# Kernel tuning notes

Hardware: AMD Instinct MI355X
Metric: run time of the kernel (lower is better)

The kernel has to match this reference:

```python
import jax, jax.numpy as jnp
import numpy as np

ACT_BIT = 3
W_BIT = 2


def fake_quant(x, bits):
    """Symmetric uniform fake-quantization to `bits` bits (dequantized values)."""
    qmax = float((1 << (bits - 1)) - 1)
    scale = jnp.max(jnp.abs(x)) / qmax
    scale = jnp.where(scale == 0, jnp.ones_like(scale), scale)
    return jnp.clip(jnp.round(x / scale), -qmax, qmax) * scale


def setup_inputs() -> dict:
    key = jax.random.key(0)
    kA, kX, kWi, kWo = jax.random.split(key, 4)
    N, D_IN, D_H, D_OUT = 8192, 128, 64, 16
    A = jax.random.normal(kA, (N, N), dtype=jnp.float32)       # dense subgraph adjacency (binarized inside)
    X = jax.random.normal(kX, (N, D_IN), dtype=jnp.float32)    # node features
    W_in = jax.random.normal(kWi, (D_IN, D_H), dtype=jnp.float32)
    W_out = jax.random.normal(kWo, (D_H, D_OUT), dtype=jnp.float32)
    return {"A": A, "X": X, "W_in": W_in, "W_out": W_out}


def reference(A, X, W_in, W_out):
    # QGTC GCNConv_Qnt: A quantized to 1 bit, activations to act_bit, weights to w_bit.
    Aq = (A > 0).astype(A.dtype)                 # 1-bit adjacency (bit_qnt(A, 1))
    Xq = fake_quant(X, ACT_BIT)                  # X_Qnt
    Wi = fake_quant(W_in, W_BIT)                 # weight_Qnt
    Wo = fake_quant(W_out, W_BIT)
    # Layer 1: mm_v1(X, W_in) then mm_v1(A, .) with output re-quantized to act_bit
    h = Aq @ (Xq @ Wi)                           # [N, D_H]
    hq = fake_quant(h, ACT_BIT)
    # Layer 2 (output layer)
    out = Aq @ (hq @ Wo)                         # [N, D_OUT]
    return out
```

## Files before the change

### kernel.cpp

```cpp
#include <hip/hip_runtime.h>

#define NN 8192
#define DIN 128
#define DH 64
#define DOUT 16
#define KS 16

typedef _Float16 half8 __attribute__((ext_vector_type(8)));
typedef float f32x4 __attribute__((ext_vector_type(4)));

#define OFF_SC    0u
#define OFF_PART  256u
#define OFF_WIQ   2048u
#define OFF_WOQ   34816u
#define OFF_YT    65536u
#define OFF_RT    1114112u
#define OFF_HF    1376256u
#define OFF_BITS  3473408u
#define OFF_P1    11862016u
#define OFF_P2    45416448u

__device__ __forceinline__ float getscale(const unsigned* sc, int idx, float qmax) {
  float s = __uint_as_float(sc[idx]) / qmax;
  return (s == 0.0f) ? 1.0f : s;
}

__device__ __forceinline__ half8 expand8(unsigned bb) {
  uint4 w;
  w.x = ((bb & 1u)  ? 0x3C00u : 0u) | ((bb & 2u)   ? 0x3C000000u : 0u);
  w.y = ((bb & 4u)  ? 0x3C00u : 0u) | ((bb & 8u)   ? 0x3C000000u : 0u);
  w.z = ((bb & 16u) ? 0x3C00u : 0u) | ((bb & 32u)  ? 0x3C000000u : 0u);
  w.w = ((bb & 64u) ? 0x3C00u : 0u) | ((bb & 128u) ? 0x3C000000u : 0u);
  return __builtin_bit_cast(half8, w);
}

__global__ __launch_bounds__(256) void k_scales(const float* __restrict__ X,
                                                const float* __restrict__ Wi,
                                                const float* __restrict__ Wo,
                                                unsigned* part) {
  __shared__ float red[256];
  int t = threadIdx.x, b = blockIdx.x;
  float m = 0.0f;
  if (b < 240) {
    for (int i = b * 256 + t; i < NN * DIN; i += 240 * 256) m = fmaxf(m, fabsf(X[i]));
  } else if (b == 240) {
    for (int i = t; i < DIN * DH; i += 256) m = fmaxf(m, fabsf(Wi[i]));
  } else {
    for (int i = t; i < DH * DOUT; i += 256) m = fmaxf(m, fabsf(Wo[i]));
  }
  red[t] = m; __syncthreads();
  for (int s = 128; s > 0; s >>= 1) {
    if (t < s) red[t] = fmaxf(red[t], red[t + s]);
    __syncthreads();
  }
  if (t == 0) part[b] = __float_as_uint(red[0]);
}

__global__ __launch_bounds__(256) void k_quantW(const float* __restrict__ Wi,
                                                const float* __restrict__ Wo,
                                                const unsigned* __restrict__ part,
                                                unsigned* sc,
                                                float* __restrict__ Wiq,
                                                float* __restrict__ Woq) {
  __shared__ float red[256];
  int t = threadIdx.x;
  red[t] = (t < 240) ? __uint_as_float(part[t]) : 0.0f;
  __syncthreads();
  for (int s = 128; s > 0; s >>= 1) {
    if (t < s) red[t] = fmaxf(red[t], red[t + s]);
    __syncthreads();
  }
  if (t == 0) {
    sc[0] = __float_as_uint(red[0]);
    sc[1] = part[240];
    sc[2] = part[241];
    sc[3] = 0u;
  }
  float swi = __uint_as_float(part[240]); swi = (swi == 0.0f) ? 1.0f : swi;
  float swo = __uint_as_float(part[241]); swo = (swo == 0.0f) ? 1.0f : swo;
  for (int i = t; i < DIN * DH; i += 256) {
    float q = rintf(Wi[i] / swi);
    Wiq[i] = fminf(fmaxf(q, -1.0f), 1.0f);
  }
  for (int i = t; i < DH * DOUT; i += 256) {
    float q = rintf(Wo[i] / swo);
    Woq[i] = fminf(fmaxf(q, -1.0f), 1.0f);
  }
}

__global__ __launch_bounds__(256) void k_bitsY(const float* __restrict__ A,
                                               const float* __restrict__ X,
                                               const float* __restrict__ Wiq,
                                               const unsigned* __restrict__ sc,
                                               unsigned char* __restrict__ bits,
                                               _Float16* __restrict__ YT) {
  __shared__ float Xs[8][129];
  __shared__ float Ws[DIN][DH];
  const int t = threadIdx.x, bx = blockIdx.x;
  if (bx < 4096) {
    const int lane = t & 63, warp = t >> 6;
    const size_t wbase = ((size_t)bx * 4 + warp) * 4096;
    const float* ap = A + wbase + lane;
    unsigned char* bp = bits + (wbase >> 3);
    const int l8 = lane & 7;
#pragma unroll
    for (int g = 0; g < 8; ++g) {
      float x0 = ap[g * 512 + 0 * 64];
      float x1 = ap[g * 512 + 1 * 64];
      float x2 = ap[g * 512 + 2 * 64];
      float x3 = ap[g * 512 + 3 * 64];
      float x4 = ap[g * 512 + 4 * 64];
      float x5 = ap[g * 512 + 5 * 64];
      float x6 = ap[g * 512 + 6 * 64];
      float x7 = ap[g * 512 + 7 * 64];
      unsigned long long m0 = __ballot(x0 > 0.0f);
      unsigned long long m1 = __ballot(x1 > 0.0f);
      unsigned long long m2 = __ballot(x2 > 0.0f);
      unsigned long long m3 = __ballot(x3 > 0.0f);
      unsigned long long m4 = __ballot(x4 > 0.0f);
      unsigned long long m5 = __ballot(x5 > 0.0f);
      unsigned long long m6 = __ballot(x6 > 0.0f);
      unsigned long long m7 = __ballot(x7 > 0.0f);
      unsigned long long mine = m0;
      mine = (l8 == 1) ? m1 : mine;
      mine = (l8 == 2) ? m2 : mine;
      mine = (l8 == 3) ? m3 : mine;
      mine = (l8 == 4) ? m4 : mine;
      mine = (l8 == 5) ? m5 : mine;
      mine = (l8 == 6) ? m6 : mine;
      mine = (l8 == 7) ? m7 : mine;
      if (lane < 8) *(unsigned long long*)(bp + g * 64 + l8 * 8) = mine;
    }
    return;
  }
  float sx = getscale(sc, 0, 3.0f);
  const int by = bx - 4096;
  const int k0 = by * 8;
  for (int i = t; i < 8 * DIN; i += 256) {
    int r = i >> 7, c = i & 127;
    float q = rintf(X[(size_t)(k0 + r) * DIN + c] / sx);
    Xs[r][c] = fminf(fmaxf(q, -3.0f), 3.0f);
  }
  for (int i = t; i < DIN * DH; i += 256) Ws[i >> 6][i & 63] = Wiq[i];
  __syncthreads();
  const int r = t & 7, jp = t >> 3, j = jp * 2;
  float a0 = 0.0f, a1 = 0.0f;
  for (int n = 0; n < DIN; ++n) {
    float xv = Xs[r][n];
    a0 = fmaf(xv, Ws[n][j], a0);
    a1 = fmaf(xv, Ws[n][j + 1], a1);
  }
  YT[(size_t)j * NN + k0 + r]       = (_Float16)a0;
  YT[(size_t)(j + 1) * NN + k0 + r] = (_Float16)a1;
}

__global__ __launch_bounds__(256) void k_gemm1(const unsigned char* __restrict__ bits,
                                               const _Float16* __restrict__ YT,
                                               float* __restrict__ P1) {
  __shared__ __align__(16) char Bs[64 * 128];
  const int t = threadIdx.x, lane = t & 63, warp = t >> 6;
  const int row0 = blockIdx.x * 128;
  const int split = blockIdx.y;
  const int l15 = lane & 15, lq = lane >> 4;
  const int sh8 = lq * 8;

  f32x4 acc[2][4] = {};

  const int bn = t >> 2, bp = t & 3;
  const _Float16* bsrc = YT + (size_t)bn * NN + split * 512 + bp * 16;
  char* bdst0 = &Bs[bn * 128 + ((bp * 32) ^ ((bn & 7) << 4))];
  char* bdst1 = &Bs[bn * 128 + ((bp * 32 + 16) ^ ((bn & 7) << 4))];

  const unsigned char* brow0 = bits + (size_t)(row0 + warp * 32 + l15) * 1024 + split * 64;
  const unsigned char* brow1 = brow0 + 16 * 1024;

  uint4 breg0 = *(const uint4*)(bsrc);
  uint4 breg1 = *(const uint4*)(bsrc + 8);

  for (int it = 0; it < 8; ++it) {
    __syncthreads();
    *(uint4*)bdst0 = breg0;
    *(uint4*)bdst1 = breg1;
    if (it < 7) {
      breg0 = *(const uint4*)(bsrc + (it + 1) * 64);
      breg1 = *(const uint4*)(bsrc + (it + 1) * 64 + 8);
    }
    uint2 w0 = *(const uint2*)(brow0 + it * 8);
    uint2 w1 = *(const uint2*)(brow1 + it * 8);
    __syncthreads();
#pragma unroll
    for (int kk = 0; kk < 2; ++kk) {
      half8 af0 = expand8(((kk ? w0.y : w0.x) >> sh8) & 0xffu);
      half8 af1 = expand8(((kk ? w1.y : w1.x) >> sh8) & 0xffu);
#pragma unroll
      for (int n = 0; n < 4; ++n) {
        half8 bf = *(const half8*)(&Bs[(n * 16 + l15) * 128 +
                                       ((lq * 16 + kk * 64) ^ ((l15 & 7) << 4))]);
        acc[0][n] = __builtin_amdgcn_mfma_f32_16x16x32_f16(af0, bf, acc[0][n], 0, 0, 0);
        acc[1][n] = __builtin_amdgcn_mfma_f32_16x16x32_f16(af1, bf, acc[1][n], 0, 0, 0);
      }
    }
  }
  const int r4 = lq * 4;
#pragma unroll
  for (int mf = 0; mf < 2; ++mf) {
#pragma unroll
    for (int n = 0; n < 4; ++n) {
#pragma unroll
      for (int i = 0; i < 4; ++i) {
        int rr = row0 + warp * 32 + mf * 16 + r4 + i;
        int cc = n * 16 + l15;
        P1[((size_t)split * NN + rr) * DH + cc] = acc[mf][n][i];
      }
    }
  }
}

__global__ __launch_bounds__(256) void k_h2(const float* __restrict__ P1,
                                            unsigned* sc, float* __restrict__ hf) {
  float sxw = getscale(sc, 0, 3.0f) * getscale(sc, 1, 1.0f);
  int idx = blockIdx.x * 256 + threadIdx.x;
  const float4* p = (const float4*)P1;
  float4 s = {0, 0, 0, 0};
#pragma unroll
  for (int sp = 0; sp < KS; ++sp) {
    float4 v = p[(size_t)sp * (NN * DH / 4) + idx];
    s.x += v.x; s.y += v.y; s.z += v.z; s.w += v.w;
  }
  s.x *= sxw; s.y *= sxw; s.z *= sxw; s.w *= sxw;
  ((float4*)hf)[idx] = s;
  float m = fmaxf(fmaxf(fabsf(s.x), fabsf(s.y)), fmaxf(fabsf(s.z), fabsf(s.w)));
  __shared__ float red[256];
  red[threadIdx.x] = m; __syncthreads();
  for (int st = 128; st > 0; st >>= 1) {
    if (threadIdx.x < st) red[threadIdx.x] = fmaxf(red[threadIdx.x], red[threadIdx.x + st]);
    __syncthreads();
  }
  if (threadIdx.x == 0) atomicMax(&sc[3], __float_as_uint(red[0]));
}

__global__ __launch_bounds__(256) void k_R(const float* __restrict__ hf,
                                           const float* __restrict__ Woq,
                                           const unsigned* __restrict__ sc,
                                           _Float16* __restrict__ RT) {
  __shared__ float WoS[DH][DOUT];
  float sh = getscale(sc, 3, 3.0f);
  int t = threadIdx.x;
  for (int i = t; i < DH * DOUT; i += 256) WoS[i >> 4][i & 15] = Woq[i];
  __syncthreads();
  int i = blockIdx.x * 16 + (t & 15), j = t >> 4;
  const float4* hp = (const float4*)(hf + (size_t)i * DH);
  float acc = 0.0f;
#pragma unroll 4
  for (int nb = 0; nb < 16; ++nb) {
    float4 h4 = hp[nb];
    float q;
    q = fminf(fmaxf(rintf(h4.x / sh), -3.0f), 3.0f); acc = fmaf(q, WoS[nb * 4 + 0][j], acc);
    q = fminf(fmaxf(rintf(h4.y / sh), -3.0f), 3.0f); acc = fmaf(q, WoS[nb * 4 + 1][j], acc);
    q = fminf(fmaxf(rintf(h4.z / sh), -3.0f), 3.0f); acc = fmaf(q, WoS[nb * 4 + 2][j], acc);
    q = fminf(fmaxf(rintf(h4.w / sh), -3.0f), 3.0f); acc = fmaf(q, WoS[nb * 4 + 3][j], acc);
  }
  RT[(size_t)j * NN + i] = (_Float16)acc;
}

__global__ __launch_bounds__(256) void k_gemm2(const unsigned char* __restrict__ bits,
                                               const _Float16* __restrict__ RT,
                                               float* __restrict__ P2) {
  __shared__ __align__(16) char Rs[16 * 1024];
  const int t = threadIdx.x, lane = t & 63, warp = t >> 6;
  const int row0 = blockIdx.x * 64;
  const int split = blockIdx.y;
  const int l15 = lane & 15, lq = lane >> 4;
  const int sh8 = lq * 8;

  {
    const int rr = t >> 4, cb = (t & 15) * 64;
    const uint4* src = (const uint4*)(RT + (size_t)rr * NN + split * 512 + (t & 15) * 32);
    char* base = &Rs[rr * 1024];
    const int sw = (rr & 7) << 4;
#pragma unroll
    for (int u = 0; u < 4; ++u) *(uint4*)(&base[(cb + u * 16) ^ sw]) = src[u];
  }
  __syncthreads();

  const unsigned char* brow = bits + (size_t)(row0 + warp * 16 + l15) * 1024 + split * 64;
  f32x4 acc = {};
  const int rsw = (l15 & 7) << 4;
#pragma unroll
  for (int it = 0; it < 8; ++it) {
    uint2 w = *(const uint2*)(brow + it * 8);
#pragma unroll
    for (int kk = 0; kk < 2; ++kk) {
      half8 af = expand8(((kk ? w.y : w.x) >> sh8) & 0xffu);
      half8 bf = *(const half8*)(&Rs[l15 * 1024 + ((it * 128 + lq * 16 + kk * 64) ^ rsw)]);
      acc = __builtin_amdgcn_mfma_f32_16x16x32_f16(af, bf, acc, 0, 0, 0);
    }
  }
  const int r4 = lq * 4;
#pragma unroll
  for (int i = 0; i < 4; ++i) {
    int rr = row0 + warp * 16 + r4 + i;
    P2[((size_t)split * NN + rr) * DOUT + l15] = acc[i];
  }
}

__global__ __launch_bounds__(256) void k_out(const float* __restrict__ P2,
                                             const unsigned* __restrict__ sc,
                                             float* __restrict__ out) {
  float s = getscale(sc, 3, 3.0f) * getscale(sc, 2, 1.0f);
  int idx = blockIdx.x * 256 + threadIdx.x;
  const float4* p = (const float4*)P2;
  float4 acc = {0, 0, 0, 0};
#pragma unroll
  for (int sp = 0; sp < KS; ++sp) {
    float4 v = p[(size_t)sp * (NN * DOUT / 4) + idx];
    acc.x += v.x; acc.y += v.y; acc.z += v.z; acc.w += v.w;
  }
  acc.x *= s; acc.y *= s; acc.z *= s; acc.w *= s;
  ((float4*)out)[idx] = acc;
}

extern "C" void kernel_launch(void* const* d_in, const int* in_sizes, int n_in,
                              void* d_out, int out_size, void* d_ws, size_t ws_size,
                              hipStream_t stream) {
  const float* A  = (const float*)d_in[0];
  const float* X  = (const float*)d_in[1];
  const float* Wi = (const float*)d_in[2];
  const float* Wo = (const float*)d_in[3];
  char* ws = (char*)d_ws;
  unsigned* sc        = (unsigned*)(ws + OFF_SC);
  unsigned* part      = (unsigned*)(ws + OFF_PART);
  float* Wiq          = (float*)(ws + OFF_WIQ);
  float* Woq          = (float*)(ws + OFF_WOQ);
  _Float16* YT        = (_Float16*)(ws + OFF_YT);
  _Float16* RT        = (_Float16*)(ws + OFF_RT);
  float* hf           = (float*)(ws + OFF_HF);
  unsigned char* bits = (unsigned char*)(ws + OFF_BITS);
  float* P1           = (float*)(ws + OFF_P1);
  float* P2           = (float*)(ws + OFF_P2);
  float* out          = (float*)d_out;

  k_scales<<<242, 256, 0, stream>>>(X, Wi, Wo, part);
  k_quantW<<<1, 256, 0, stream>>>(Wi, Wo, part, sc, Wiq, Woq);
  k_bitsY<<<5120, 256, 0, stream>>>(A, X, Wiq, sc, bits, YT);
  k_gemm1<<<dim3(NN / 128, KS), 256, 0, stream>>>(bits, YT, P1);
  k_h2<<<NN * DH / 1024, 256, 0, stream>>>(P1, sc, hf);
  k_R<<<NN / 16, 256, 0, stream>>>(hf, Woq, sc, RT);
  k_gemm2<<<dim3(NN / 64, KS), 256, 0, stream>>>(bits, RT, P2);
  k_out<<<NN * DOUT / 1024, 256, 0, stream>>>(P2, sc, out);
}
```

Before: 129.9 us.

## Fuse scale/bit-packing passes, vectorize A binarization, drop split-K partials in second GEMM

A's sign-bit packing now runs in the same launch as the absmax scale reduction, using float4 loads with a different bit ordering. To match that ordering, a column permutation (permk) is applied when writing YT and RT. Weight quantization is folded into the consumer kernels, which removes the k_quantW launch and its workspace buffers. The second GEMM now computes a full-K reduction per block, with an intra-block LDS reduction, and writes scaled output directly, which eliminates the P2 partials and the k_out kernel. The first GEMM's split-K is halved, which lowers partial traffic but costs parallelism. The trade is fewer launches and less global traffic against longer per-block K loops and direct global B-fragment loads in gemm2.

```diff
diff --git a/kernel.cpp b/kernel.cpp
--- a/kernel.cpp
+++ b/kernel.cpp
@@ -4,21 +4,23 @@
 #define DIN 128
 #define DH 64
 #define DOUT 16
-#define KS 16
+#define KS 8
 
 typedef _Float16 half8 __attribute__((ext_vector_type(8)));
 typedef float f32x4 __attribute__((ext_vector_type(4)));
 
 #define OFF_SC    0u
 #define OFF_PART  256u
-#define OFF_WIQ   2048u
-#define OFF_WOQ   34816u
 #define OFF_YT    65536u
 #define OFF_RT    1114112u
 #define OFF_HF    1376256u
 #define OFF_BITS  3473408u
 #define OFF_P1    11862016u
-#define OFF_P2    45416448u
+
+__device__ __forceinline__ int permk(int k) {
+  int e = k & 255;
+  return (k & ~255) | (((e & 3) << 6) | (e >> 2));
+}
 
 __device__ __forceinline__ float getscale(const unsigned* sc, int idx, float qmax) {
   float s = __uint_as_float(sc[idx]) / qmax;
@@ -34,17 +36,40 @@
   return __builtin_bit_cast(half8, w);
 }
 
-__global__ __launch_bounds__(256) void k_scales(const float* __restrict__ X,
-                                                const float* __restrict__ Wi,
-                                                const float* __restrict__ Wo,
-                                                unsigned* part) {
+__global__ __launch_bounds__(256) void k_scalesbits(const float* __restrict__ A,
+                                                    const float* __restrict__ X,
+                                                    const float* __restrict__ Wi,
+                                                    const float* __restrict__ Wo,
+                                                    unsigned char* __restrict__ bits,
+                                                    unsigned* part, unsigned* sc) {
+  const int t = threadIdx.x, bx = blockIdx.x;
+  if (bx < 4096) {
+    const int lane = t & 63, warp = t >> 6;
+    const size_t wbase = ((size_t)bx * 4 + warp) * 4096;
+    const float4* ap = (const float4*)(A + wbase) + lane;
+    unsigned char* bp = bits + (wbase >> 3);
+#pragma unroll
+    for (int g = 0; g < 16; ++g) {
+      float4 v = ap[g * 64];
+      unsigned long long m0 = __ballot(v.x > 0.0f);
+      unsigned long long m1 = __ballot(v.y > 0.0f);
+      unsigned long long m2 = __ballot(v.z > 0.0f);
+      unsigned long long m3 = __ballot(v.w > 0.0f);
+      unsigned long long lo = (lane & 1) ? m1 : m0;
+      unsigned long long hi = (lane & 1) ? m3 : m2;
+      unsigned long long word = (lane & 2) ? hi : lo;
+      if (lane < 4) *(unsigned long long*)(bp + g * 32 + lane * 8) = word;
+    }
+    return;
+  }
   __shared__ float red[256];
-  int t = threadIdx.x, b = blockIdx.x;
+  const int b = bx - 4096;
   float m = 0.0f;
   if (b < 240) {
     for (int i = b * 256 + t; i < NN * DIN; i += 240 * 256) m = fmaxf(m, fabsf(X[i]));
   } else if (b == 240) {
     for (int i = t; i < DIN * DH; i += 256) m = fmaxf(m, fabsf(Wi[i]));
+    if (t == 0) sc[3] = 0u;
   } else {
     for (int i = t; i < DH * DOUT; i += 256) m = fmaxf(m, fabsf(Wo[i]));
   }
@@ -56,92 +81,36 @@
   if (t == 0) part[b] = __float_as_uint(red[0]);
 }
 
-__global__ __launch_bounds__(256) void k_quantW(const float* __restrict__ Wi,
-                                                const float* __restrict__ Wo,
-                                                const unsigned* __restrict__ part,
-                                                unsigned* sc,
-                                                float* __restrict__ Wiq,
-                                                float* __restrict__ Woq) {
+__global__ __launch_bounds__(256) void k_Y(const float* __restrict__ X,
+                                           const float* __restrict__ Wi,
+                                           const unsigned* __restrict__ part,
+                                           unsigned* sc,
+                                           _Float16* __restrict__ YT) {
   __shared__ float red[256];
-  int t = threadIdx.x;
+  __shared__ float Xs[8][129];
+  __shared__ float Ws[DIN][DH];
+  const int t = threadIdx.x;
   red[t] = (t < 240) ? __uint_as_float(part[t]) : 0.0f;
   __syncthreads();
   for (int s = 128; s > 0; s >>= 1) {
     if (t < s) red[t] = fmaxf(red[t], red[t + s]);
     __syncthreads();
   }
-  if (t == 0) {
-    sc[0] = __float_as_uint(red[0]);
-    sc[1] = part[240];
-    sc[2] = part[241];
-    sc[3] = 0u;
-  }
+  float sxraw = red[0];
+  float sx = sxraw / 3.0f; sx = (sx == 0.0f) ? 1.0f : sx;
   float swi = __uint_as_float(part[240]); swi = (swi == 0.0f) ? 1.0f : swi;
-  float swo = __uint_as_float(part[241]); swo = (swo == 0.0f) ? 1.0f : swo;
-  for (int i = t; i < DIN * DH; i += 256) {
-    float q = rintf(Wi[i] / swi);
-    Wiq[i] = fminf(fmaxf(q, -1.0f), 1.0f);
-  }
-  for (int i = t; i < DH * DOUT; i += 256) {
-    float q = rintf(Wo[i] / swo);
-    Woq[i] = fminf(fmaxf(q, -1.0f), 1.0f);
-  }
-}
-
-__global__ __launch_bounds__(256) void k_bitsY(const float* __restrict__ A,
-                                               const float* __restrict__ X,
-                                               const float* __restrict__ Wiq,
-                                               const unsigned* __restrict__ sc,
-                                               unsigned char* __restrict__ bits,
-                                               _Float16* __restrict__ YT) {
-  __shared__ float Xs[8][129];
-  __shared__ float Ws[DIN][DH];
-  const int t = threadIdx.x, bx = blockIdx.x;
-  if (bx < 4096) {
-    const int lane = t & 63, warp = t >> 6;
-    const size_t wbase = ((size_t)bx * 4 + warp) * 4096;
-    const float* ap = A + wbase + lane;
-    unsigned char* bp = bits + (wbase >> 3);
-    const int l8 = lane & 7;
-#pragma unroll
-    for (int g = 0; g < 8; ++g) {
-      float x0 = ap[g * 512 + 0 * 64];
-      float x1 = ap[g * 512 + 1 * 64];
-      float x2 = ap[g * 512 + 2 * 64];
-      float x3 = ap[g * 512 + 3 * 64];
-      float x4 = ap[g * 512 + 4 * 64];
-      float x5 = ap[g * 512 + 5 * 64];
-      float x6 = ap[g * 512 + 6 * 64];
-      float x7 = ap[g * 512 + 7 * 64];
-      unsigned long long m0 = __ballot(x0 > 0.0f);
-      unsigned long long m1 = __ballot(x1 > 0.0f);
-      unsigned long long m2 = __ballot(x2 > 0.0f);
-      unsigned long long m3 = __ballot(x3 > 0.0f);
-      unsigned long long m4 = __ballot(x4 > 0.0f);
-      unsigned long long m5 = __ballot(x5 > 0.0f);
-      unsigned long long m6 = __ballot(x6 > 0.0f);
-      unsigned long long m7 = __ballot(x7 > 0.0f);
-      unsigned long long mine = m0;
-      mine = (l8 == 1) ? m1 : mine;
-      mine = (l8 == 2) ? m2 : mine;
-      mine = (l8 == 3) ? m3 : mine;
-      mine = (l8 == 4) ? m4 : mine;
-      mine = (l8 == 5) ? m5 : mine;
-      mine = (l8 == 6) ? m6 : mine;
-      mine = (l8 == 7) ? m7 : mine;
-      if (lane < 8) *(unsigned long long*)(bp + g * 64 + l8 * 8) = mine;
-    }
-    return;
-  }
-  float sx = getscale(sc, 0, 3.0f);
-  const int by = bx - 4096;
-  const int k0 = by * 8;
+  if (blockIdx.x == 0 && t == 0) sc[0] = __float_as_uint(sxraw);
+  const int k0 = blockIdx.x * 8;
+  __syncthreads();
   for (int i = t; i < 8 * DIN; i += 256) {
     int r = i >> 7, c = i & 127;
     float q = rintf(X[(size_t)(k0 + r) * DIN + c] / sx);
     Xs[r][c] = fminf(fmaxf(q, -3.0f), 3.0f);
   }
-  for (int i = t; i < DIN * DH; i += 256) Ws[i >> 6][i & 63] = Wiq[i];
+  for (int i = t; i < DIN * DH; i += 256) {
+    float q = rintf(Wi[i] / swi);
+    Ws[i >> 6][i & 63] = fminf(fmaxf(q, -1.0f), 1.0f);
+  }
   __syncthreads();
   const int r = t & 7, jp = t >> 3, j = jp * 2;
   float a0 = 0.0f, a1 = 0.0f;
@@ -150,8 +119,9 @@
     a0 = fmaf(xv, Ws[n][j], a0);
     a1 = fmaf(xv, Ws[n][j + 1], a1);
   }
-  YT[(size_t)j * NN + k0 + r]       = (_Float16)a0;
-  YT[(size_t)(j + 1) * NN + k0 + r] = (_Float16)a1;
+  const int kp = permk(k0 + r);
+  YT[(size_t)j * NN + kp]       = (_Float16)a0;
+  YT[(size_t)(j + 1) * NN + kp] = (_Float16)a1;
 }
 
 __global__ __launch_bounds__(256) void k_gemm1(const unsigned char* __restrict__ bits,
@@ -167,21 +137,21 @@
   f32x4 acc[2][4] = {};
 
   const int bn = t >> 2, bp = t & 3;
-  const _Float16* bsrc = YT + (size_t)bn * NN + split * 512 + bp * 16;
+  const _Float16* bsrc = YT + (size_t)bn * NN + split * 1024 + bp * 16;
   char* bdst0 = &Bs[bn * 128 + ((bp * 32) ^ ((bn & 7) << 4))];
   char* bdst1 = &Bs[bn * 128 + ((bp * 32 + 16) ^ ((bn & 7) << 4))];
 
-  const unsigned char* brow0 = bits + (size_t)(row0 + warp * 32 + l15) * 1024 + split * 64;
+  const unsigned char* brow0 = bits + (size_t)(row0 + warp * 32 + l15) * 1024 + split * 128;
   const unsigned char* brow1 = brow0 + 16 * 1024;
 
   uint4 breg0 = *(const uint4*)(bsrc);
   uint4 breg1 = *(const uint4*)(bsrc + 8);
 
-  for (int it = 0; it < 8; ++it) {
+  for (int it = 0; it < 16; ++it) {
     __syncthreads();
     *(uint4*)bdst0 = breg0;
     *(uint4*)bdst1 = breg1;
-    if (it < 7) {
+    if (it < 15) {
       breg0 = *(const uint4*)(bsrc + (it + 1) * 64);
       breg1 = *(const uint4*)(bsrc + (it + 1) * 64 + 8);
     }
@@ -217,8 +187,11 @@
 }
 
 __global__ __launch_bounds__(256) void k_h2(const float* __restrict__ P1,
+                                            const unsigned* __restrict__ part,
                                             unsigned* sc, float* __restrict__ hf) {
-  float sxw = getscale(sc, 0, 3.0f) * getscale(sc, 1, 1.0f);
+  float sx = getscale(sc, 0, 3.0f);
+  float swi = __uint_as_float(part[240]); swi = (swi == 0.0f) ? 1.0f : swi;
+  float sxw = sx * swi;
   int idx = blockIdx.x * 256 + threadIdx.x;
   const float4* p = (const float4*)P1;
   float4 s = {0, 0, 0, 0};
@@ -240,13 +213,18 @@
 }
 
 __global__ __launch_bounds__(256) void k_R(const float* __restrict__ hf,
-                                           const float* __restrict__ Woq,
+                                           const float* __restrict__ Wo,
+                                           const unsigned* __restrict__ part,
                                            const unsigned* __restrict__ sc,
                                            _Float16* __restrict__ RT) {
   __shared__ float WoS[DH][DOUT];
   float sh = getscale(sc, 3, 3.0f);
+  float swo = __uint_as_float(part[241]); swo = (swo == 0.0f) ? 1.0f : swo;
   int t = threadIdx.x;
-  for (int i = t; i < DH * DOUT; i += 256) WoS[i >> 4][i & 15] = Woq[i];
+  for (int i = t; i < DH * DOUT; i += 256) {
+    float q = rintf(Wo[i] / swo);
+    WoS[i >> 4][i & 15] = fminf(fmaxf(q, -1.0f), 1.0f);
+  }
   __syncthreads();
   int i = blockIdx.x * 16 + (t & 15), j = t >> 4;
   const float4* hp = (const float4*)(hf + (size_t)i * DH);
@@ -260,64 +238,50 @@
     q = fminf(fmaxf(rintf(h4.z / sh), -3.0f), 3.0f); acc = fmaf(q, WoS[nb * 4 + 2][j], acc);
     q = fminf(fmaxf(rintf(h4.w / sh), -3.0f), 3.0f); acc = fmaf(q, WoS[nb * 4 + 3][j], acc);
   }
-  RT[(size_t)j * NN + i] = (_Float16)acc;
+  RT[(size_t)j * NN + permk(i)] = (_Float16)acc;
 }
 
 __global__ __launch_bounds__(256) void k_gemm2(const unsigned char* __restrict__ bits,
                                                const _Float16* __restrict__ RT,
-                                               float* __restrict__ P2) {
-  __shared__ __align__(16) char Rs[16 * 1024];
+                                               const unsigned* __restrict__ part,
+                                               const unsigned* __restrict__ sc,
+                                               float* __restrict__ out) {
+  __shared__ float red2[3][16][16];
   const int t = threadIdx.x, lane = t & 63, warp = t >> 6;
-  const int row0 = blockIdx.x * 64;
-  const int split = blockIdx.y;
+  const int row0 = blockIdx.x * 16;
   const int l15 = lane & 15, lq = lane >> 4;
   const int sh8 = lq * 8;
 
-  {
-    const int rr = t >> 4, cb = (t & 15) * 64;
-    const uint4* src = (const uint4*)(RT + (size_t)rr * NN + split * 512 + (t & 15) * 32);
-    char* base = &Rs[rr * 1024];
-    const int sw = (rr & 7) << 4;
-#pragma unroll
-    for (int u = 0; u < 4; ++u) *(uint4*)(&base[(cb + u * 16) ^ sw]) = src[u];
-  }
-  __syncthreads();
-
-  const unsigned char* brow = bits + (size_t)(row0 + warp * 16 + l15) * 1024 + split * 64;
+  const unsigned char* brow = bits + (size_t)(row0 + l15) * 1024 + warp * 256;
+  const _Float16* rrow = RT + (size_t)l15 * NN + warp * 2048 + lq * 8;
+
   f32x4 acc = {};
-  const int rsw = (l15 & 7) << 4;
-#pragma unroll
-  for (int it = 0; it < 8; ++it) {
+#pragma unroll 8
+  for (int it = 0; it < 32; ++it) {
     uint2 w = *(const uint2*)(brow + it * 8);
 #pragma unroll
     for (int kk = 0; kk < 2; ++kk) {
       half8 af = expand8(((kk ? w.y : w.x) >> sh8) & 0xffu);
-      half8 bf = *(const half8*)(&Rs[l15 * 1024 + ((it * 128 + lq * 16 + kk * 64) ^ rsw)]);
+      half8 bf = *(const half8*)(rrow + it * 64 + kk * 32);
       acc = __builtin_amdgcn_mfma_f32_16x16x32_f16(af, bf, acc, 0, 0, 0);
     }
   }
-  const int r4 = lq * 4;
-#pragma unroll
-  for (int i = 0; i < 4; ++i) {
-    int rr = row0 + warp * 16 + r4 + i;
-    P2[((size_t)split * NN + rr) * DOUT + l15] = acc[i];
-  }
-}
-
-__global__ __launch_bounds__(256) void k_out(const float* __restrict__ P2,
-                                             const unsigned* __restrict__ sc,
-                                             float* __restrict__ out) {
-  float s = getscale(sc, 3, 3.0f) * getscale(sc, 2, 1.0f);
-  int idx = blockIdx.x * 256 + threadIdx.x;
-  const float4* p = (const float4*)P2;
-  float4 acc = {0, 0, 0, 0};
-#pragma unroll
-  for (int sp = 0; sp < KS; ++sp) {
-    float4 v = p[(size_t)sp * (NN * DOUT / 4) + idx];
-    acc.x += v.x; acc.y += v.y; acc.z += v.z; acc.w += v.w;
-  }
-  acc.x *= s; acc.y *= s; acc.z *= s; acc.w *= s;
-  ((float4*)out)[idx] = acc;
+  if (warp > 0) {
+#pragma unroll
+    for (int i = 0; i < 4; ++i) red2[warp - 1][lq * 4 + i][l15] = acc[i];
+  }
+  __syncthreads();
+  if (warp == 0) {
+    float sh = getscale(sc, 3, 3.0f);
+    float swo = __uint_as_float(part[241]); swo = (swo == 0.0f) ? 1.0f : swo;
+    float s = sh * swo;
+#pragma unroll
+    for (int i = 0; i < 4; ++i) {
+      int r = lq * 4 + i;
+      float v = acc[i] + red2[0][r][l15] + red2[1][r][l15] + red2[2][r][l15];
+      out[(size_t)(row0 + r) * DOUT + l15] = v * s;
+    }
+  }
 }
 
 extern "C" void kernel_launch(void* const* d_in, const int* in_sizes, int n_in,
@@ -330,22 +294,17 @@
   char* ws = (char*)d_ws;
   unsigned* sc        = (unsigned*)(ws + OFF_SC);
   unsigned* part      = (unsigned*)(ws + OFF_PART);
-  float* Wiq          = (float*)(ws + OFF_WIQ);
-  float* Woq          = (float*)(ws + OFF_WOQ);
   _Float16* YT        = (_Float16*)(ws + OFF_YT);
   _Float16* RT        = (_Float16*)(ws + OFF_RT);
   float* hf           = (float*)(ws + OFF_HF);
   unsigned char* bits = (unsigned char*)(ws + OFF_BITS);
   float* P1           = (float*)(ws + OFF_P1);
-  float* P2           = (float*)(ws + OFF_P2);
   float* out          = (float*)d_out;
 
-  k_scales<<<242, 256, 0, stream>>>(X, Wi, Wo, part);
-  k_quantW<<<1, 256, 0, stream>>>(Wi, Wo, part, sc, Wiq, Woq);
-  k_bitsY<<<5120, 256, 0, stream>>>(A, X, Wiq, sc, bits, YT);
+  k_scalesbits<<<4338, 256, 0, stream>>>(A, X, Wi, Wo, bits, part, sc);
+  k_Y<<<1024, 256, 0, stream>>>(X, Wi, part, sc, YT);
   k_gemm1<<<dim3(NN / 128, KS), 256, 0, stream>>>(bits, YT, P1);
-  k_h2<<<NN * DH / 1024, 256, 0, stream>>>(P1, sc, hf);
-  k_R<<<NN / 16, 256, 0, stream>>>(hf, Woq, sc, RT);
-  k_gemm2<<<dim3(NN / 64, KS), 256, 0, stream>>>(bits, RT, P2);
-  k_out<<<NN * DOUT / 1024, 256, 0, stream>>>(P2, sc, out);
-}
+  k_h2<<<NN * DH / 1024, 256, 0, stream>>>(P1, part, sc, hf);
+  k_R<<<NN / 16, 256, 0, stream>>>(hf, Wo, part, sc, RT);
+  k_gemm2<<<NN / 16, 256, 0, stream>>>(bits, RT, part, sc, out);
+}
```

Measured after the change: 125.7 us. 3.2% less time.
